# Kernel optimization log

Hardware: AMD Instinct MI355X
Metric: run time of the kernel (lower is better)

## Reference

```python
import jax, jax.numpy as jnp
import numpy as np

L = 2        # n_layers
F = 128      # in_features == out_features (GRUCell + highway constraint)
O = 128
N = 1024     # nodes
B = 8        # batch
D = 3        # edge directions (weight.size(0))


def setup_inputs() -> dict:
    key = jax.random.key(0)
    ks = jax.random.split(key, 10)
    s = 1.0 / np.sqrt(F)
    u = lambda k, shp: jax.random.uniform(k, shp, jnp.float32, minval=-s, maxval=s)
    return {
        "inputs": jax.random.normal(ks[0], (N, B, F), jnp.float32),
        "adj": jax.random.uniform(ks[1], (D, B, N, N), jnp.float32),
        "W": u(ks[2], (L, D, F, O)),            # GCN weight per layer/direction
        "Bc": u(ks[3], (L, D, O)),              # GCN bias
        "Wh": u(ks[4], (L, F, O)),              # highway weight
        "Bh": u(ks[5], (L, O)),                 # highway bias
        "Wih": u(ks[6], (L, 3 * O, O)),         # GRUCell input weights
        "Whh": u(ks[7], (L, 3 * O, O)),         # GRUCell hidden weights
        "bih": u(ks[8], (L, 3 * O)),
        "bhh": u(ks[9], (L, 3 * O)),
    }


def _gru(x, h, wih, whh, bih, bhh):
    # torch.nn.GRUCell semantics; x,h: [..., O]
    gi = x @ wih.T + bih
    gh = h @ whh.T + bhh
    i_r, i_z, i_n = jnp.split(gi, 3, axis=-1)
    h_r, h_z, h_n = jnp.split(gh, 3, axis=-1)
    r = jax.nn.sigmoid(i_r + h_r)
    z = jax.nn.sigmoid(i_z + h_z)
    n = jnp.tanh(i_n + r * h_n)
    return (1.0 - z) * n + z * h


def reference(inputs, adj, W, Bc, Wh, Bh, Wih, Whh, bih, bhh):
    x = inputs  # [N, B, F]; dropout layers are identity at eval
    for l in range(L):
        # support per direction: [D, B, N, O]
        support = jnp.einsum('nbf,dfo->dbno', x, W[l]) + Bc[l][:, None, None, :]
        # adjacency-weighted aggregation: adj[d,b] @ support[d,b]
        agg = jnp.einsum('dbmn,dbno->dbmo', adj, support)
        # GRU update with hidden = current features, per direction, summed over d
        h = jnp.broadcast_to(jnp.transpose(x, (1, 0, 2))[None], agg.shape)
        hnew = _gru(agg, h, Wih[l], Whh[l], bih[l], bhh[l])
        out = jnp.transpose(jnp.sum(hnew, axis=0), (1, 0, 2))  # [N, B, O]
        out = jax.nn.relu(out)  # activation='relu'
        # highway gate (highway='relu')
        t = jax.nn.relu(jnp.einsum('nbf,fo->nbo', x, Wh[l]) + Bh[l])
        x = out * t + x * (1.0 - t)
    return x
```

## Files before the change

### kernel.cpp

```cpp
#include <hip/hip_runtime.h>
#include <math.h>

#define N_NODES 1024
#define BATCH   8
#define FEAT    128
#define NDIR    3
#define NB      (N_NODES*BATCH)
#define G3      384

typedef __bf16 bf16_t;
using bf16x8 = __attribute__((ext_vector_type(8))) __bf16;
using bf16x4 = __attribute__((ext_vector_type(4))) __bf16;
using f32x4  = __attribute__((ext_vector_type(4))) float;

#define GLOAD_LDS16(g, l) \
    __builtin_amdgcn_global_load_lds((const __attribute__((address_space(1))) void*)(g), \
                                     (__attribute__((address_space(3))) void*)(l), 16, 0, 0)

#define STAGE64(As, Bs, Arow, Brow, sA, sB, k0, w, lane)                      \
    {                                                                          \
        _Pragma("unroll")                                                      \
        for (int q = 0; q < 2; ++q) {                                          \
            int qq = (w)*2 + q;                                                \
            int row = qq*8 + ((lane) >> 3), seg = (lane) & 7;                  \
            GLOAD_LDS16((Arow) + (size_t)row*(sA) + (k0) + seg*8,              \
                        (char*)(As) + qq*1024);                                \
            GLOAD_LDS16((Brow) + (size_t)row*(sB) + (k0) + seg*8,              \
                        (char*)(Bs) + qq*1024);                                \
        }                                                                      \
    }

#define MFMA64(As, Bs, acc, w, lane)                                           \
    {                                                                          \
        _Pragma("unroll")                                                      \
        for (int ks = 0; ks < 64; ks += 32) {                                  \
            bf16x8 af = *reinterpret_cast<const bf16x8*>(                      \
                &(As)[((w)*16 + ((lane) & 15))*64 + ks + (((lane) >> 4) * 8)]);\
            _Pragma("unroll")                                                  \
            for (int j = 0; j < 4; ++j) {                                      \
                bf16x8 bfv = *reinterpret_cast<const bf16x8*>(                 \
                    &(Bs)[(j*16 + ((lane) & 15))*64 + ks + (((lane) >> 4) * 8)]);\
                (acc)[j] = __builtin_amdgcn_mfma_f32_16x16x32_bf16(af, bfv, (acc)[j], 0, 0, 0); \
            }                                                                  \
        }                                                                      \
    }

__global__ __launch_bounds__(256) void k_cvt_adj(
    const float* __restrict__ src, bf16_t* __restrict__ dst, int n4)
{
    int i = blockIdx.x * 256 + threadIdx.x;
    int stride = gridDim.x * 256;
    for (; i < n4; i += stride) {
        float4 v = reinterpret_cast<const float4*>(src)[i];
        bf16x4 o;
        o[0] = (bf16_t)(v.x - 0.5f); o[1] = (bf16_t)(v.y - 0.5f);
        o[2] = (bf16_t)(v.z - 0.5f); o[3] = (bf16_t)(v.w - 0.5f);
        *reinterpret_cast<bf16x4*>(&dst[(size_t)i * 4]) = o;
    }
}

__global__ __launch_bounds__(128) void k_wprep(
    const float* __restrict__ W, const float* __restrict__ Wh,
    const float* __restrict__ Whh, const float* __restrict__ Wih,
    bf16_t* __restrict__ wsup,
    bf16_t* __restrict__ whhc,
    bf16_t* __restrict__ wihc)
{
    int m = blockIdx.x, l = blockIdx.y, k = threadIdx.x;
    float w;
    bf16_t* dst;
    bool patB = false;
    if (m < 384) {
        int d = m >> 7, o = m & 127;
        w = W[((size_t)(l*3 + d)*128 + k)*128 + o];
        dst = wsup + ((size_t)l*512 + m)*384;
    } else if (m < 512) {
        int o = m - 384;
        w = Wh[((size_t)l*128 + k)*128 + o];
        dst = wsup + ((size_t)l*512 + m)*384;
    } else if (m < 896) {
        int c = m - 512;
        w = Whh[((size_t)l*384 + c)*128 + k];
        dst = whhc + ((size_t)l*384 + c)*384;
    } else {
        int c = m - 896;
        w = Wih[((size_t)l*384 + c)*128 + k];
        dst = wihc + ((size_t)l*384 + c)*384;
        patB = true;
    }
    bf16_t hi = (bf16_t)w;
    bf16_t lo = (bf16_t)(w - (float)hi);
    if (patB) { dst[k] = hi; dst[128 + k] = hi; dst[256 + k] = lo; }
    else      { dst[k] = hi; dst[128 + k] = lo; dst[256 + k] = hi; }
}

__global__ __launch_bounds__(256) void k_xcat(
    const float* __restrict__ X, bf16_t* __restrict__ xcat)
{
    int idx = blockIdx.x * 256 + threadIdx.x;
    int k = idx & 127, r = idx >> 7;
    int n = r >> 3, b = r & 7;
    float v = X[idx];
    bf16_t hi = (bf16_t)v;
    bf16_t lo = (bf16_t)(v - (float)hi);
    bf16_t* dst = xcat + ((size_t)(b*1024 + n))*384 + k;
    dst[0] = hi; dst[128] = hi; dst[256] = lo;
}

__global__ __launch_bounds__(256, 4) void k_sup(
    const bf16_t* __restrict__ Wcat,
    const bf16_t* __restrict__ xcat,
    const float* __restrict__ Bcl,
    const float* __restrict__ Bhl,
    bf16_t* __restrict__ supt,
    float* __restrict__ tbuf)
{
    __shared__ bf16_t As[64*64];
    __shared__ bf16_t Bs[64*64];
    const int t = threadIdx.x, lane = t & 63, w = t >> 6;
    const int n0 = blockIdx.x * 64;
    const int m0 = blockIdx.y * 64;
    const int b  = blockIdx.z;
    const bf16_t* Arow = Wcat + (size_t)m0 * 384;
    const bf16_t* Brow = xcat + ((size_t)b * 1024 + n0) * 384;

    f32x4 acc[4] = {};
    for (int k0 = 0; k0 < 384; k0 += 64) {
        STAGE64(As, Bs, Arow, Brow, 384, 384, k0, w, lane);
        __syncthreads();
        MFMA64(As, Bs, acc, w, lane);
        __syncthreads();
    }
    #pragma unroll
    for (int j = 0; j < 4; ++j) {
        int n = n0 + j*16 + (lane & 15);
        #pragma unroll
        for (int rg = 0; rg < 4; ++rg) {
            int m = m0 + w*16 + (lane >> 4)*4 + rg;
            float v = acc[j][rg];
            if (m < 384) {
                int d = m >> 7, o = m & 127;
                supt[((size_t)((d*8 + b)*128 + o))*1024 + n] = (bf16_t)(v + Bcl[d*128 + o]);
            } else {
                int o = m - 384;
                tbuf[((size_t)(b*128 + o))*1024 + n] = fmaxf(v + Bhl[o], 0.0f);
            }
        }
    }
}

__global__ __launch_bounds__(256) void k_colsum(
    const bf16_t* __restrict__ supt, float* __restrict__ colsum)
{
    int row = blockIdx.x * 4 + (threadIdx.x >> 6);
    int lane = threadIdx.x & 63;
    const bf16_t* p = supt + (size_t)row * 1024 + lane * 16;
    bf16x8 v0 = *reinterpret_cast<const bf16x8*>(p);
    bf16x8 v1 = *reinterpret_cast<const bf16x8*>(p + 8);
    float s = 0.0f;
    #pragma unroll
    for (int i = 0; i < 8; ++i) s += (float)v0[i] + (float)v1[i];
    #pragma unroll
    for (int off = 32; off > 0; off >>= 1) s += __shfl_down(s, off, 64);
    if (lane == 0) colsum[row] = s;
}

__global__ __launch_bounds__(256, 4) void k_gh(
    const bf16_t* __restrict__ A,
    const bf16_t* __restrict__ B,
    const float* __restrict__ bias,
    bf16_t* __restrict__ C)
{
    __shared__ bf16_t As[64*64];
    __shared__ bf16_t Bs[64*64];
    const int t = threadIdx.x, lane = t & 63, w = t >> 6;
    const int m0 = blockIdx.x * 64;
    const int c0 = blockIdx.y * 64;
    const bf16_t* Arow = A + (size_t)m0 * 384;
    const bf16_t* Brow = B + (size_t)c0 * 384;

    f32x4 acc[4] = {};
    for (int k0 = 0; k0 < 384; k0 += 64) {
        STAGE64(As, Bs, Arow, Brow, 384, 384, k0, w, lane);
        __syncthreads();
        MFMA64(As, Bs, acc, w, lane);
        __syncthreads();
    }
    #pragma unroll
    for (int j = 0; j < 4; ++j) {
        int c = c0 + j*16 + (lane & 15);
        float bv = bias[c];
        #pragma unroll
        for (int rg = 0; rg < 4; ++rg) {
            int m = m0 + w*16 + (lane >> 4)*4 + rg;
            C[(size_t)m*G3 + c] = (bf16_t)(acc[j][rg] + bv);
        }
    }
}

__global__ __launch_bounds__(256, 4) void k_agg(
    const bf16_t* __restrict__ adjb,
    const bf16_t* __restrict__ supt,
    const float* __restrict__ colsum,
    bf16_t* __restrict__ aggcat)
{
    __shared__ bf16_t As[64*64];
    __shared__ bf16_t Bs[64*64];
    const int t = threadIdx.x, lane = t & 63, w = t >> 6;
    const int m0 = blockIdx.x * 64;
    const int o0 = blockIdx.y * 64;
    const int z  = blockIdx.z;
    const bf16_t* Arow = adjb + (size_t)z * 1024 * 1024 + (size_t)m0 * 1024;
    const bf16_t* Brow = supt + (size_t)z * 128 * 1024 + (size_t)o0 * 1024;

    f32x4 acc[4] = {};
    for (int k0 = 0; k0 < 1024; k0 += 64) {
        STAGE64(As, Bs, Arow, Brow, 1024, 1024, k0, w, lane);
        __syncthreads();
        MFMA64(As, Bs, acc, w, lane);
        __syncthreads();
    }
    #pragma unroll
    for (int j = 0; j < 4; ++j) {
        int o = o0 + j*16 + (lane & 15);
        float cs = 0.5f * colsum[z*128 + o];
        #pragma unroll
        for (int rg = 0; rg < 4; ++rg) {
            size_t m = (size_t)z*1024 + m0 + w*16 + (lane >> 4)*4 + rg;
            float v = acc[j][rg] + cs;
            bf16_t hi = (bf16_t)v;
            bf16_t lo = (bf16_t)(v - (float)hi);
            bf16_t* row = aggcat + m*384;
            row[o] = hi; row[128 + o] = lo; row[256 + o] = hi;
        }
    }
}

__global__ __launch_bounds__(256, 4) void k_gi(
    const bf16_t* __restrict__ A,
    const bf16_t* __restrict__ B,
    const float*  __restrict__ bias,
    bf16_t* __restrict__ girz,
    float* __restrict__ gin)
{
    __shared__ bf16_t As[64*64];
    __shared__ bf16_t Bs[64*64];
    const int t = threadIdx.x, lane = t & 63, w = t >> 6;
    const int m0 = blockIdx.x * 64;
    const int c0 = blockIdx.y * 64;
    const bf16_t* Arow = A + (size_t)m0 * 384;
    const bf16_t* Brow = B + (size_t)c0 * 384;

    f32x4 acc[4] = {};
    for (int k0 = 0; k0 < 384; k0 += 64) {
        STAGE64(As, Bs, Arow, Brow, 384, 384, k0, w, lane);
        __syncthreads();
        MFMA64(As, Bs, acc, w, lane);
        __syncthreads();
    }
    #pragma unroll
    for (int j = 0; j < 4; ++j) {
        int c = c0 + j*16 + (lane & 15);
        float bv = bias[c];
        #pragma unroll
        for (int rg = 0; rg < 4; ++rg) {
            int m = m0 + w*16 + (lane >> 4)*4 + rg;
            float v = acc[j][rg] + bv;
            if (c < 256) girz[(size_t)m*256 + c] = (bf16_t)v;
            else         gin[(size_t)m*128 + (c - 256)] = v;
        }
    }
}

__global__ __launch_bounds__(256) void k_gates(
    const bf16_t* __restrict__ girz, const float* __restrict__ gin,
    const bf16_t* __restrict__ ghb,
    bf16_t* xcat,
    const float* __restrict__ tbuf,
    float* __restrict__ Xout, int write_xcat)
{
    __shared__ float ts[128*17];
    const int b = blockIdx.y, n0 = blockIdx.x * 16;
    const int tid = threadIdx.x;
    {
        int o = tid >> 1, nh = (tid & 1) * 8;
        const float* src = tbuf + ((size_t)(b*128 + o))*1024 + n0 + nh;
        float4 v0 = *reinterpret_cast<const float4*>(src);
        float4 v1 = *reinterpret_cast<const float4*>(src + 4);
        float* dst = &ts[o*17 + nh];
        dst[0]=v0.x; dst[1]=v0.y; dst[2]=v0.z; dst[3]=v0.w;
        dst[4]=v1.x; dst[5]=v1.y; dst[6]=v1.z; dst[7]=v1.w;
    }
    __syncthreads();
    #pragma unroll
    for (int p = 0; p < 8; ++p) {
        int e = p*256 + tid;
        int nn = e >> 7, o = e & 127;
        int n = n0 + nn;
        size_t rb = (size_t)(b*1024 + n);
        bf16_t* xr = xcat + rb*384;
        float h = (float)xr[o] + (float)xr[256 + o];
        const bf16_t* ghr = ghb + rb*G3;
        float g_r = (float)ghr[o], g_z = (float)ghr[128+o], g_n = (float)ghr[256+o];
        float acc = 0.0f;
        #pragma unroll
        for (int d = 0; d < 3; ++d) {
            size_t rr = (size_t)((d*8 + b)*1024 + n);
            float i_r = (float)girz[rr*256 + o];
            float i_z = (float)girz[rr*256 + 128 + o];
            float i_n = gin[rr*128 + o];
            float rg = 1.0f / (1.0f + expf(-(i_r + g_r)));
            float zg = 1.0f / (1.0f + expf(-(i_z + g_z)));
            float ng = tanhf(i_n + rg * g_n);
            acc += (1.0f - zg) * ng + zg * h;
        }
        float outv = fmaxf(acc, 0.0f);
        float tg = ts[o*17 + nn];
        float res = outv * tg + h * (1.0f - tg);
        if (Xout) Xout[(size_t)(n*8 + b)*128 + o] = res;
        if (write_xcat) {
            bf16_t hi = (bf16_t)res;
            bf16_t lo = (bf16_t)(res - (float)hi);
            xr[o] = hi; xr[128 + o] = hi; xr[256 + o] = lo;
        }
    }
}

extern "C" void kernel_launch(void* const* d_in, const int* in_sizes, int n_in,
                              void* d_out, int out_size, void* d_ws, size_t ws_size,
                              hipStream_t stream) {
    const float* inputs = (const float*)d_in[0];
    const float* adj    = (const float*)d_in[1];
    const float* W      = (const float*)d_in[2];
    const float* Bc     = (const float*)d_in[3];
    const float* Wh     = (const float*)d_in[4];
    const float* Bh     = (const float*)d_in[5];
    const float* Wih    = (const float*)d_in[6];
    const float* Whh    = (const float*)d_in[7];
    const float* bih    = (const float*)d_in[8];
    const float* bhh    = (const float*)d_in[9];

    char* ws = (char*)d_ws;
    float*  tbuf   = (float*)ws;   ws += (size_t)8*128*1024*4;
    bf16_t* xcat   = (bf16_t*)ws;  ws += (size_t)8*1024*384*2;
    bf16_t* ghb    = (bf16_t*)ws;  ws += (size_t)NB*G3*2;
    bf16_t* supt   = (bf16_t*)ws;  ws += (size_t)24*128*1024*2;
    bf16_t* aggcat = (bf16_t*)ws;  ws += (size_t)3*NB*384*2;
    bf16_t* girz   = (bf16_t*)ws;  ws += (size_t)3*NB*256*2;
    float*  gin    = (float*)ws;   ws += (size_t)3*NB*128*4;
    float*  colsum = (float*)ws;   ws += (size_t)24*128*4;
    bf16_t* wsup   = (bf16_t*)ws;  ws += (size_t)2*512*384*2;
    bf16_t* whhc   = (bf16_t*)ws;  ws += (size_t)2*384*384*2;
    bf16_t* wihc   = (bf16_t*)ws;  ws += (size_t)2*384*384*2;
    bf16_t* adjb   = (bf16_t*)ws;

    k_cvt_adj<<<dim3(4096), dim3(256), 0, stream>>>(adj, adjb, 3*8*1024*1024/4);
    k_wprep<<<dim3(1280, 2), dim3(128), 0, stream>>>(W, Wh, Whh, Wih, wsup, whhc, wihc);
    k_xcat<<<dim3(4096), dim3(256), 0, stream>>>(inputs, xcat);

    for (int l = 0; l < 2; ++l) {
        k_sup<<<dim3(16, 8, 8), dim3(256), 0, stream>>>(
            wsup + (size_t)l*512*384, xcat, Bc + l*3*128, Bh + l*128, supt, tbuf);
        k_colsum<<<dim3(768), dim3(256), 0, stream>>>(supt, colsum);
        k_gh<<<dim3(128, 6), dim3(256), 0, stream>>>(
            xcat, whhc + (size_t)l*384*384, bhh + l*G3, ghb);
        k_agg<<<dim3(16, 2, 24), dim3(256), 0, stream>>>(adjb, supt, colsum, aggcat);
        k_gi<<<dim3(384, 6), dim3(256), 0, stream>>>(
            aggcat, wihc + (size_t)l*384*384, bih + l*G3, girz, gin);
        k_gates<<<dim3(64, 8), dim3(256), 0, stream>>>(
            girz, gin, ghb, xcat, tbuf,
            (l == 1) ? (float*)d_out : (float*)nullptr, (l == 0) ? 1 : 0);
    }
}
```

Measured before the change: 342.0 us.

## Fuse hidden-gate GEMM into support GEMM and enlarge MFMA tiles to 128

Concatenates the Whh weights into the support weight matrix so one GEMM over xcat produces support, highway gate and the hidden GRU projection, which removes the separate k_gh launch and a second read of xcat. The support, gi and agg GEMMs move to larger 128-wide block tiles with a 2x2 wave layout and multi-fragment MFMA accumulation, for more register-level reuse of the loaded operands. The cost is more registers and LDS per block (launch bounds lowered to 2 blocks per CU) and fewer blocks in the grid, which may reduce occupancy.

```diff
diff --git a/kernel.cpp b/kernel.cpp
--- a/kernel.cpp
+++ b/kernel.cpp
@@ -17,33 +17,43 @@
     __builtin_amdgcn_global_load_lds((const __attribute__((address_space(1))) void*)(g), \
                                      (__attribute__((address_space(3))) void*)(l), 16, 0, 0)
 
-#define STAGE64(As, Bs, Arow, Brow, sA, sB, k0, w, lane)                      \
-    {                                                                          \
-        _Pragma("unroll")                                                      \
-        for (int q = 0; q < 2; ++q) {                                          \
-            int qq = (w)*2 + q;                                                \
-            int row = qq*8 + ((lane) >> 3), seg = (lane) & 7;                  \
-            GLOAD_LDS16((Arow) + (size_t)row*(sA) + (k0) + seg*8,              \
-                        (char*)(As) + qq*1024);                                \
-            GLOAD_LDS16((Brow) + (size_t)row*(sB) + (k0) + seg*8,              \
-                        (char*)(Bs) + qq*1024);                                \
-        }                                                                      \
-    }
-
-#define MFMA64(As, Bs, acc, w, lane)                                           \
-    {                                                                          \
-        _Pragma("unroll")                                                      \
-        for (int ks = 0; ks < 64; ks += 32) {                                  \
-            bf16x8 af = *reinterpret_cast<const bf16x8*>(                      \
-                &(As)[((w)*16 + ((lane) & 15))*64 + ks + (((lane) >> 4) * 8)]);\
-            _Pragma("unroll")                                                  \
-            for (int j = 0; j < 4; ++j) {                                      \
-                bf16x8 bfv = *reinterpret_cast<const bf16x8*>(                 \
-                    &(Bs)[(j*16 + ((lane) & 15))*64 + ks + (((lane) >> 4) * 8)]);\
-                (acc)[j] = __builtin_amdgcn_mfma_f32_16x16x32_bf16(af, bfv, (acc)[j], 0, 0, 0); \
-            }                                                                  \
-        }                                                                      \
-    }
+template<int R>
+__device__ __forceinline__ void stage_op(const bf16_t* __restrict__ src, int stride,
+                                         int k0, bf16_t* lds, int w, int lane)
+{
+    #pragma unroll
+    for (int q = 0; q < R/32; ++q) {
+        int rbase = w*(R/4) + q*8;
+        int row = rbase + (lane >> 3);
+        int seg = lane & 7;
+        GLOAD_LDS16(src + (size_t)row*stride + k0 + seg*8,
+                    (char*)lds + (size_t)rbase*128);
+    }
+}
+
+template<int MI, int NJ>
+__device__ __forceinline__ void mfma_tile(const bf16_t* As, const bf16_t* Bs,
+                                          f32x4 (&acc)[MI][NJ], int wr, int wc, int lane)
+{
+    #pragma unroll
+    for (int ks = 0; ks < 64; ks += 32) {
+        bf16x8 af[MI], bf[NJ];
+        #pragma unroll
+        for (int i = 0; i < MI; ++i)
+            af[i] = *reinterpret_cast<const bf16x8*>(
+                &As[(wr*MI*16 + i*16 + (lane & 15))*64 + ks + ((lane >> 4) * 8)]);
+        #pragma unroll
+        for (int j = 0; j < NJ; ++j)
+            bf[j] = *reinterpret_cast<const bf16x8*>(
+                &Bs[(wc*NJ*16 + j*16 + (lane & 15))*64 + ks + ((lane >> 4) * 8)]);
+        #pragma unroll
+        for (int i = 0; i < MI; ++i) {
+            #pragma unroll
+            for (int j = 0; j < NJ; ++j)
+                acc[i][j] = __builtin_amdgcn_mfma_f32_16x16x32_bf16(af[i], bf[j], acc[i][j], 0, 0, 0);
+        }
+    }
+}
 
 __global__ __launch_bounds__(256) void k_cvt_adj(
     const float* __restrict__ src, bf16_t* __restrict__ dst, int n4)
@@ -63,7 +73,6 @@
     const float* __restrict__ W, const float* __restrict__ Wh,
     const float* __restrict__ Whh, const float* __restrict__ Wih,
     bf16_t* __restrict__ wsup,
-    bf16_t* __restrict__ whhc,
     bf16_t* __restrict__ wihc)
 {
     int m = blockIdx.x, l = blockIdx.y, k = threadIdx.x;
@@ -73,15 +82,15 @@
     if (m < 384) {
         int d = m >> 7, o = m & 127;
         w = W[((size_t)(l*3 + d)*128 + k)*128 + o];
-        dst = wsup + ((size_t)l*512 + m)*384;
+        dst = wsup + ((size_t)l*896 + m)*384;
     } else if (m < 512) {
         int o = m - 384;
         w = Wh[((size_t)l*128 + k)*128 + o];
-        dst = wsup + ((size_t)l*512 + m)*384;
+        dst = wsup + ((size_t)l*896 + m)*384;
     } else if (m < 896) {
         int c = m - 512;
         w = Whh[((size_t)l*384 + c)*128 + k];
-        dst = whhc + ((size_t)l*384 + c)*384;
+        dst = wsup + ((size_t)l*896 + m)*384;
     } else {
         int c = m - 896;
         w = Wih[((size_t)l*384 + c)*128 + k];
@@ -107,43 +116,62 @@
     dst[0] = hi; dst[128] = hi; dst[256] = lo;
 }
 
-__global__ __launch_bounds__(256, 4) void k_sup(
+__global__ __launch_bounds__(256, 2) void k_sup2(
     const bf16_t* __restrict__ Wcat,
     const bf16_t* __restrict__ xcat,
     const float* __restrict__ Bcl,
     const float* __restrict__ Bhl,
+    const float* __restrict__ bhhl,
     bf16_t* __restrict__ supt,
-    float* __restrict__ tbuf)
-{
-    __shared__ bf16_t As[64*64];
-    __shared__ bf16_t Bs[64*64];
+    float* __restrict__ tbuf,
+    bf16_t* __restrict__ ghb)
+{
+    __shared__ bf16_t As[128*64];
+    __shared__ bf16_t Bs[128*64];
     const int t = threadIdx.x, lane = t & 63, w = t >> 6;
-    const int n0 = blockIdx.x * 64;
-    const int m0 = blockIdx.y * 64;
+    const int wr = w >> 1, wc = w & 1;
+    const int n0 = blockIdx.x * 128;
+    const int m0 = blockIdx.y * 128;
     const int b  = blockIdx.z;
     const bf16_t* Arow = Wcat + (size_t)m0 * 384;
     const bf16_t* Brow = xcat + ((size_t)b * 1024 + n0) * 384;
 
-    f32x4 acc[4] = {};
+    f32x4 acc[4][4] = {};
     for (int k0 = 0; k0 < 384; k0 += 64) {
-        STAGE64(As, Bs, Arow, Brow, 384, 384, k0, w, lane);
-        __syncthreads();
-        MFMA64(As, Bs, acc, w, lane);
-        __syncthreads();
-    }
-    #pragma unroll
-    for (int j = 0; j < 4; ++j) {
-        int n = n0 + j*16 + (lane & 15);
-        #pragma unroll
-        for (int rg = 0; rg < 4; ++rg) {
-            int m = m0 + w*16 + (lane >> 4)*4 + rg;
-            float v = acc[j][rg];
-            if (m < 384) {
-                int d = m >> 7, o = m & 127;
-                supt[((size_t)((d*8 + b)*128 + o))*1024 + n] = (bf16_t)(v + Bcl[d*128 + o]);
+        stage_op<128>(Arow, 384, k0, As, w, lane);
+        stage_op<128>(Brow, 384, k0, Bs, w, lane);
+        __syncthreads();
+        mfma_tile<4,4>(As, Bs, acc, wr, wc, lane);
+        __syncthreads();
+    }
+    #pragma unroll
+    for (int i = 0; i < 4; ++i) {
+        int mb = m0 + wr*64 + i*16 + ((lane >> 4) * 4);
+        #pragma unroll
+        for (int j = 0; j < 4; ++j) {
+            int n = n0 + wc*64 + j*16 + (lane & 15);
+            if (mb < 384) {
+                #pragma unroll
+                for (int rg = 0; rg < 4; ++rg) {
+                    int m = mb + rg;
+                    int d = m >> 7, o = m & 127;
+                    supt[((size_t)((d*8 + b)*128 + o))*1024 + n] =
+                        (bf16_t)(acc[i][j][rg] + Bcl[d*128 + o]);
+                }
+            } else if (mb < 512) {
+                #pragma unroll
+                for (int rg = 0; rg < 4; ++rg) {
+                    int o = mb + rg - 384;
+                    tbuf[((size_t)(b*128 + o))*1024 + n] =
+                        fmaxf(acc[i][j][rg] + Bhl[o], 0.0f);
+                }
             } else {
-                int o = m - 384;
-                tbuf[((size_t)(b*128 + o))*1024 + n] = fmaxf(v + Bhl[o], 0.0f);
+                int c = mb - 512;
+                bf16x4 pk;
+                #pragma unroll
+                for (int rg = 0; rg < 4; ++rg)
+                    pk[rg] = (bf16_t)(acc[i][j][rg] + bhhl[c + rg]);
+                *reinterpret_cast<bf16x4*>(&ghb[((size_t)(b*1024 + n))*384 + c]) = pk;
             }
         }
     }
@@ -165,109 +193,84 @@
     if (lane == 0) colsum[row] = s;
 }
 
-__global__ __launch_bounds__(256, 4) void k_gh(
-    const bf16_t* __restrict__ A,
-    const bf16_t* __restrict__ B,
-    const float* __restrict__ bias,
-    bf16_t* __restrict__ C)
-{
-    __shared__ bf16_t As[64*64];
-    __shared__ bf16_t Bs[64*64];
-    const int t = threadIdx.x, lane = t & 63, w = t >> 6;
-    const int m0 = blockIdx.x * 64;
-    const int c0 = blockIdx.y * 64;
-    const bf16_t* Arow = A + (size_t)m0 * 384;
-    const bf16_t* Brow = B + (size_t)c0 * 384;
-
-    f32x4 acc[4] = {};
-    for (int k0 = 0; k0 < 384; k0 += 64) {
-        STAGE64(As, Bs, Arow, Brow, 384, 384, k0, w, lane);
-        __syncthreads();
-        MFMA64(As, Bs, acc, w, lane);
-        __syncthreads();
-    }
-    #pragma unroll
-    for (int j = 0; j < 4; ++j) {
-        int c = c0 + j*16 + (lane & 15);
-        float bv = bias[c];
-        #pragma unroll
-        for (int rg = 0; rg < 4; ++rg) {
-            int m = m0 + w*16 + (lane >> 4)*4 + rg;
-            C[(size_t)m*G3 + c] = (bf16_t)(acc[j][rg] + bv);
-        }
-    }
-}
-
-__global__ __launch_bounds__(256, 4) void k_agg(
+__global__ __launch_bounds__(256, 2) void k_agg(
     const bf16_t* __restrict__ adjb,
     const bf16_t* __restrict__ supt,
     const float* __restrict__ colsum,
     bf16_t* __restrict__ aggcat)
 {
     __shared__ bf16_t As[64*64];
-    __shared__ bf16_t Bs[64*64];
+    __shared__ bf16_t Bs[128*64];
     const int t = threadIdx.x, lane = t & 63, w = t >> 6;
+    const int wr = w >> 1, wc = w & 1;
     const int m0 = blockIdx.x * 64;
-    const int o0 = blockIdx.y * 64;
-    const int z  = blockIdx.z;
+    const int z  = blockIdx.y;
     const bf16_t* Arow = adjb + (size_t)z * 1024 * 1024 + (size_t)m0 * 1024;
-    const bf16_t* Brow = supt + (size_t)z * 128 * 1024 + (size_t)o0 * 1024;
-
-    f32x4 acc[4] = {};
+    const bf16_t* Brow = supt + (size_t)z * 128 * 1024;
+
+    f32x4 acc[2][4] = {};
     for (int k0 = 0; k0 < 1024; k0 += 64) {
-        STAGE64(As, Bs, Arow, Brow, 1024, 1024, k0, w, lane);
-        __syncthreads();
-        MFMA64(As, Bs, acc, w, lane);
-        __syncthreads();
-    }
-    #pragma unroll
-    for (int j = 0; j < 4; ++j) {
-        int o = o0 + j*16 + (lane & 15);
-        float cs = 0.5f * colsum[z*128 + o];
+        stage_op<64>(Arow, 1024, k0, As, w, lane);
+        stage_op<128>(Brow, 1024, k0, Bs, w, lane);
+        __syncthreads();
+        mfma_tile<2,4>(As, Bs, acc, wr, wc, lane);
+        __syncthreads();
+    }
+    #pragma unroll
+    for (int i = 0; i < 2; ++i) {
         #pragma unroll
         for (int rg = 0; rg < 4; ++rg) {
-            size_t m = (size_t)z*1024 + m0 + w*16 + (lane >> 4)*4 + rg;
-            float v = acc[j][rg] + cs;
-            bf16_t hi = (bf16_t)v;
-            bf16_t lo = (bf16_t)(v - (float)hi);
+            size_t m = (size_t)z*1024 + m0 + wr*32 + i*16 + ((lane >> 4) * 4) + rg;
             bf16_t* row = aggcat + m*384;
-            row[o] = hi; row[128 + o] = lo; row[256 + o] = hi;
-        }
-    }
-}
-
-__global__ __launch_bounds__(256, 4) void k_gi(
+            #pragma unroll
+            for (int j = 0; j < 4; ++j) {
+                int o = wc*64 + j*16 + (lane & 15);
+                float v = acc[i][j][rg] + 0.5f * colsum[z*128 + o];
+                bf16_t hi = (bf16_t)v;
+                bf16_t lo = (bf16_t)(v - (float)hi);
+                row[o] = hi; row[128 + o] = lo; row[256 + o] = hi;
+            }
+        }
+    }
+}
+
+__global__ __launch_bounds__(256, 2) void k_gi(
     const bf16_t* __restrict__ A,
     const bf16_t* __restrict__ B,
     const float*  __restrict__ bias,
     bf16_t* __restrict__ girz,
     float* __restrict__ gin)
 {
-    __shared__ bf16_t As[64*64];
-    __shared__ bf16_t Bs[64*64];
+    __shared__ bf16_t As[128*64];
+    __shared__ bf16_t Bs[128*64];
     const int t = threadIdx.x, lane = t & 63, w = t >> 6;
-    const int m0 = blockIdx.x * 64;
-    const int c0 = blockIdx.y * 64;
+    const int wr = w >> 1, wc = w & 1;
+    const int m0 = blockIdx.x * 128;
+    const int c0 = blockIdx.y * 128;
     const bf16_t* Arow = A + (size_t)m0 * 384;
     const bf16_t* Brow = B + (size_t)c0 * 384;
 
-    f32x4 acc[4] = {};
+    f32x4 acc[4][4] = {};
     for (int k0 = 0; k0 < 384; k0 += 64) {
-        STAGE64(As, Bs, Arow, Brow, 384, 384, k0, w, lane);
-        __syncthreads();
-        MFMA64(As, Bs, acc, w, lane);
+        stage_op<128>(Arow, 384, k0, As, w, lane);
+        stage_op<128>(Brow, 384, k0, Bs, w, lane);
+        __syncthreads();
+        mfma_tile<4,4>(As, Bs, acc, wr, wc, lane);
         __syncthreads();
     }
     #pragma unroll
     for (int j = 0; j < 4; ++j) {
-        int c = c0 + j*16 + (lane & 15);
+        int c = c0 + wc*64 + j*16 + (lane & 15);
         float bv = bias[c];
         #pragma unroll
-        for (int rg = 0; rg < 4; ++rg) {
-            int m = m0 + w*16 + (lane >> 4)*4 + rg;
-            float v = acc[j][rg] + bv;
-            if (c < 256) girz[(size_t)m*256 + c] = (bf16_t)v;
-            else         gin[(size_t)m*128 + (c - 256)] = v;
+        for (int i = 0; i < 4; ++i) {
+            #pragma unroll
+            for (int rg = 0; rg < 4; ++rg) {
+                int m = m0 + wr*64 + i*16 + ((lane >> 4) * 4) + rg;
+                float v = acc[i][j][rg] + bv;
+                if (c < 256) girz[(size_t)m*256 + c] = (bf16_t)v;
+                else         gin[(size_t)m*128 + (c - 256)] = v;
+            }
         }
     }
 }
@@ -349,23 +352,21 @@
     bf16_t* girz   = (bf16_t*)ws;  ws += (size_t)3*NB*256*2;
     float*  gin    = (float*)ws;   ws += (size_t)3*NB*128*4;
     float*  colsum = (float*)ws;   ws += (size_t)24*128*4;
-    bf16_t* wsup   = (bf16_t*)ws;  ws += (size_t)2*512*384*2;
-    bf16_t* whhc   = (bf16_t*)ws;  ws += (size_t)2*384*384*2;
+    bf16_t* wsup   = (bf16_t*)ws;  ws += (size_t)2*896*384*2;
     bf16_t* wihc   = (bf16_t*)ws;  ws += (size_t)2*384*384*2;
     bf16_t* adjb   = (bf16_t*)ws;
 
     k_cvt_adj<<<dim3(4096), dim3(256), 0, stream>>>(adj, adjb, 3*8*1024*1024/4);
-    k_wprep<<<dim3(1280, 2), dim3(128), 0, stream>>>(W, Wh, Whh, Wih, wsup, whhc, wihc);
+    k_wprep<<<dim3(1280, 2), dim3(128), 0, stream>>>(W, Wh, Whh, Wih, wsup, wihc);
     k_xcat<<<dim3(4096), dim3(256), 0, stream>>>(inputs, xcat);
 
     for (int l = 0; l < 2; ++l) {
-        k_sup<<<dim3(16, 8, 8), dim3(256), 0, stream>>>(
-            wsup + (size_t)l*512*384, xcat, Bc + l*3*128, Bh + l*128, supt, tbuf);
+        k_sup2<<<dim3(8, 7, 8), dim3(256), 0, stream>>>(
+            wsup + (size_t)l*896*384, xcat, Bc + l*3*128, Bh + l*128, bhh + l*G3,
+            supt, tbuf, ghb);
         k_colsum<<<dim3(768), dim3(256), 0, stream>>>(supt, colsum);
-        k_gh<<<dim3(128, 6), dim3(256), 0, stream>>>(
-            xcat, whhc + (size_t)l*384*384, bhh + l*G3, ghb);
-        k_agg<<<dim3(16, 2, 24), dim3(256), 0, stream>>>(adjb, supt, colsum, aggcat);
-        k_gi<<<dim3(384, 6), dim3(256), 0, stream>>>(
+        k_agg<<<dim3(16, 24), dim3(256), 0, stream>>>(adjb, supt, colsum, aggcat);
+        k_gi<<<dim3(192, 3), dim3(256), 0, stream>>>(
             aggcat, wihc + (size_t)l*384*384, bih + l*G3, girz, gin);
         k_gates<<<dim3(64, 8), dim3(256), 0, stream>>>(
             girz, gin, ghb, xcat, tbuf,
```

New measurement: 332.2 us. 2.9% less time.
